# Kernel tuning notes

Hardware: AMD Instinct MI355X
Metric: run time of the kernel (lower is better)

Reference implementation:

```python
import jax, jax.numpy as jnp
import numpy as np

WIN = 9
EPS = 1e-05


def _box_sum(x, win):
    """Depthwise win x win box-filter sum with SAME padding, via two separable 1D convs."""
    C = x.shape[1]
    pad = win // 2
    dn = ('NCHW', 'OIHW', 'NCHW')
    kh = jnp.ones((C, 1, win, 1), dtype=x.dtype)
    kw = jnp.ones((C, 1, 1, win), dtype=x.dtype)
    x = jax.lax.conv_general_dilated(x, kh, (1, 1), [(pad, pad), (0, 0)],
                                     dimension_numbers=dn, feature_group_count=C)
    x = jax.lax.conv_general_dilated(x, kw, (1, 1), [(0, 0), (pad, pad)],
                                     dimension_numbers=dn, feature_group_count=C)
    return x


def setup_inputs() -> dict:
    key = jax.random.key(0)
    k1, k2 = jax.random.split(key)
    B, C, H, W = 32, 4, 512, 512
    y_pred = jax.random.uniform(k1, (B, C, H, W), dtype=jnp.float32)
    y_true = jax.random.uniform(k2, (B, C, H, W), dtype=jnp.float32)
    return {"y_pred": y_pred, "y_true": y_true}


def reference(y_pred, y_true):
    C = y_true.shape[1]
    n = float(WIN * WIN)
    # Stack the 5 moment maps along channels -> one fused box-filter pass.
    stacked = jnp.concatenate(
        [y_true, y_pred, y_true * y_true, y_pred * y_pred, y_true * y_pred], axis=1)
    sums = _box_sum(stacked, WIN)
    sum_I, sum_J, sum_I2, sum_J2, sum_IJ = jnp.split(sums, 5, axis=1)
    mu_I = sum_I / n
    mu_J = sum_J / n
    var_I = sum_I2 / n - mu_I * mu_I
    var_J = sum_J2 / n - mu_J * mu_J
    cov_IJ = sum_IJ / n - mu_I * mu_J
    cc = cov_IJ * cov_IJ / (jnp.maximum(var_I, 0.0) * jnp.maximum(var_J, 0.0) + EPS)
    return -jnp.mean(cc)
```

## Files before the change

### kernel.cpp

```cpp
#include <hip/hip_runtime.h>


#define PAD 4
#define EPS 1e-5f

constexpr int B = 32, C = 4, H = 512, W = 512;
constexpr int ROWS = 32;
constexpr int TPB = 256;
constexpr int CPT = 2;
constexpr int SLOTS = 520;
constexpr int NCHUNK = H / ROWS;
constexpr int NBLK = B * C * NCHUNK;
constexpr int NPART = NBLK * 4;
constexpr float INV_N = 1.0f / 81.0f;

template <bool ADD>
__device__ __forceinline__ void accrow(const float* __restrict__ I,
                                       const float* __restrict__ J,
                                       int r, int x0, float s[5][CPT]) {
    const float2 vi = *(const float2*)(I + (size_t)r * W + x0);
    const float2 vj = *(const float2*)(J + (size_t)r * W + x0);
    float fi[CPT] = {vi.x, vi.y};
    float fj[CPT] = {vj.x, vj.y};
#pragma unroll
    for (int k = 0; k < CPT; ++k) {
        float a = fi[k], b = fj[k];
        if (ADD) {
            s[0][k] += a; s[1][k] += b;
            s[2][k] += a * a; s[3][k] += b * b; s[4][k] += a * b;
        } else {
            s[0][k] -= a; s[1][k] -= b;
            s[2][k] -= a * a; s[3][k] -= b * b; s[4][k] -= a * b;
        }
    }
}

__global__ __launch_bounds__(TPB) void ncc_partial(
        const float* __restrict__ y_pred, const float* __restrict__ y_true,
        float* __restrict__ partial) {
    __shared__ float vs[2][5][SLOTS];

    const int bid = blockIdx.x;
    const int chunk = bid % NCHUNK;
    const int plane = bid / NCHUNK;
    const size_t base = (size_t)plane * H * W;
    const float* I = y_true + base;
    const float* J = y_pred + base;

    const int t = threadIdx.x;
    const int x0 = t * CPT;

    if (t < 2 * PAD) {
        const int sl = (t < PAD) ? t : (512 + t);
#pragma unroll
        for (int b = 0; b < 2; ++b)
#pragma unroll
            for (int ch = 0; ch < 5; ++ch) vs[b][ch][sl] = 0.0f;
    }

    const int y0 = chunk * ROWS;

    float s[5][CPT] = {{0.f, 0.f}, {0.f, 0.f}, {0.f, 0.f}, {0.f, 0.f}, {0.f, 0.f}};

    for (int r = y0 - PAD; r < y0 + PAD; ++r) {
        if (r >= 0 && r < H) accrow<true>(I, J, r, x0, s);
    }

    float acc = 0.0f;

    for (int yo = 0; yo < ROWS; ++yo) {
        const int y = y0 + yo;
        const int rin = y + PAD;
        if (rin < H) accrow<true>(I, J, rin, x0, s);

        float (* const vb)[SLOTS] = vs[yo & 1];
#pragma unroll
        for (int ch = 0; ch < 5; ++ch)
            *(float2*)&vb[ch][x0 + PAD] = make_float2(s[ch][0], s[ch][1]);
        __syncthreads();

        float h[5][CPT];
#pragma unroll
        for (int ch = 0; ch < 5; ++ch) {
            const float* row = vb[ch];
            const float2 r0 = *(const float2*)(row + x0);
            const float2 r1 = *(const float2*)(row + x0 + 2);
            const float2 r2 = *(const float2*)(row + x0 + 4);
            const float2 r3 = *(const float2*)(row + x0 + 6);
            const float2 r4 = *(const float2*)(row + x0 + 8);
            const float s0 = r0.x + r0.y + r1.x + r1.y + r2.x + r2.y +
                             r3.x + r3.y + r4.x;
            h[ch][0] = s0;
            h[ch][1] = s0 + r4.y - r0.x;
        }

#pragma unroll
        for (int k = 0; k < CPT; ++k) {
            const float mI = h[0][k] * INV_N;
            const float mJ = h[1][k] * INV_N;
            const float vI = h[2][k] * INV_N - mI * mI;
            const float vJ = h[3][k] * INV_N - mJ * mJ;
            const float cv = h[4][k] * INV_N - mI * mJ;
            const float den = fmaxf(vI, 0.0f) * fmaxf(vJ, 0.0f) + EPS;
            acc += cv * cv / den;
        }

        const int rout = y - PAD;
        if (rout >= 0) accrow<false>(I, J, rout, x0, s);
    }

#pragma unroll
    for (int off = 32; off > 0; off >>= 1)
        acc += __shfl_down(acc, off, 64);
    if ((t & 63) == 0) partial[bid * 4 + (t >> 6)] = acc;
}

__global__ __launch_bounds__(256) void ncc_final(
        const float* __restrict__ partial, float* __restrict__ out) {
    const int t = threadIdx.x;
    float sum = 0.0f;
    for (int i = t; i < NPART; i += 256) sum += partial[i];
    __shared__ float ws[4];
#pragma unroll
    for (int off = 32; off > 0; off >>= 1)
        sum += __shfl_down(sum, off, 64);
    if ((t & 63) == 0) ws[t >> 6] = sum;
    __syncthreads();
    if (t == 0) {
        const float tot = ws[0] + ws[1] + ws[2] + ws[3];
        out[0] = -tot / (float)((long long)B * C * H * W);
    }
}

extern "C" void kernel_launch(void* const* d_in, const int* in_sizes, int n_in,
                              void* d_out, int out_size, void* d_ws, size_t ws_size,
                              hipStream_t stream) {
    const float* y_pred = (const float*)d_in[0];
    const float* y_true = (const float*)d_in[1];
    float* out = (float*)d_out;
    float* partial = (float*)d_ws;

    ncc_partial<<<NBLK, TPB, 0, stream>>>(y_pred, y_true, partial);
    ncc_final<<<1, 256, 0, stream>>>(partial, out);
}
```

Before: 115.6 us.

## Widen to 4 columns per thread, unroll rows by two with register prefetch

Each thread now handles 4 columns (128 threads per block) using float4 loads. The row loop is unrolled by two with double-buffered shared rows, and the incoming and outgoing rows are prefetched into registers ahead of use to hide global latency. The NCC math is rescaled by 81 to drop divisions and uses a fast reciprocal. Block indices are swizzled, and the per-block partial is reduced to a single value. The approximate reciprocal may slightly change precision, and the larger per-thread register footprint may lower occupancy.

New measurement: 104.0 us. 10.1% less time.

```diff
diff --git a/kernel.cpp b/kernel.cpp
--- a/kernel.cpp
+++ b/kernel.cpp
@@ -2,45 +2,80 @@
 
 
 #define PAD 4
-#define EPS 1e-5f
 
 constexpr int B = 32, C = 4, H = 512, W = 512;
 constexpr int ROWS = 32;
-constexpr int TPB = 256;
-constexpr int CPT = 2;
-constexpr int SLOTS = 520;
+constexpr int TPB = 128;
+constexpr int CPT = 4;
+constexpr int SLOTS = 528;
 constexpr int NCHUNK = H / ROWS;
 constexpr int NBLK = B * C * NCHUNK;
-constexpr int NPART = NBLK * 4;
-constexpr float INV_N = 1.0f / 81.0f;
+constexpr float EPS_N4 = 430.46721f;
 
-template <bool ADD>
-__device__ __forceinline__ void accrow(const float* __restrict__ I,
+struct RowPx { float4 i, j; };
+
+__device__ __forceinline__ void loadpx(const float* __restrict__ I,
                                        const float* __restrict__ J,
-                                       int r, int x0, float s[5][CPT]) {
-    const float2 vi = *(const float2*)(I + (size_t)r * W + x0);
-    const float2 vj = *(const float2*)(J + (size_t)r * W + x0);
-    float fi[CPT] = {vi.x, vi.y};
-    float fj[CPT] = {vj.x, vj.y};
+                                       int r, int x0, RowPx& o) {
+    o.i = *(const float4*)(I + (size_t)r * W + x0);
+    o.j = *(const float4*)(J + (size_t)r * W + x0);
+}
+
+template <int SGN>
+__device__ __forceinline__ void fold4(float s[5][4], const RowPx& R) {
+    const float fi[4] = {R.i.x, R.i.y, R.i.z, R.i.w};
+    const float fj[4] = {R.j.x, R.j.y, R.j.z, R.j.w};
 #pragma unroll
-    for (int k = 0; k < CPT; ++k) {
-        float a = fi[k], b = fj[k];
-        if (ADD) {
-            s[0][k] += a; s[1][k] += b;
-            s[2][k] += a * a; s[3][k] += b * b; s[4][k] += a * b;
+    for (int k = 0; k < 4; ++k) {
+        const float a = fi[k], b = fj[k];
+        if (SGN > 0) {
+            s[0][k] += a;        s[1][k] += b;
+            s[2][k] = fmaf(a, a, s[2][k]);
+            s[3][k] = fmaf(b, b, s[3][k]);
+            s[4][k] = fmaf(a, b, s[4][k]);
         } else {
-            s[0][k] -= a; s[1][k] -= b;
-            s[2][k] -= a * a; s[3][k] -= b * b; s[4][k] -= a * b;
+            s[0][k] -= a;        s[1][k] -= b;
+            s[2][k] = fmaf(-a, a, s[2][k]);
+            s[3][k] = fmaf(-b, b, s[3][k]);
+            s[4][k] = fmaf(-a, b, s[4][k]);
         }
     }
+}
+
+__device__ __forceinline__ float hcc(const float (* __restrict__ vb)[SLOTS],
+                                     const float s[5][4], int x0) {
+    float h[5][4];
+#pragma unroll
+    for (int ch = 0; ch < 5; ++ch) {
+        const float4 L = *(const float4*)&vb[ch][x0];
+        const float4 R = *(const float4*)&vb[ch][x0 + 8];
+        float t = L.x + L.y + L.z + L.w +
+                  s[ch][0] + s[ch][1] + s[ch][2] + s[ch][3] + R.x;
+        h[ch][0] = t;
+        t += R.y - L.x; h[ch][1] = t;
+        t += R.z - L.y; h[ch][2] = t;
+        t += R.w - L.z; h[ch][3] = t;
+    }
+    float acc = 0.0f;
+#pragma unroll
+    for (int k = 0; k < 4; ++k) {
+        const float wi = h[0][k], wj = h[1][k];
+        const float a  = fmaf(81.0f, h[4][k], -(wi * wj));
+        const float vi = fmaxf(fmaf(81.0f, h[2][k], -(wi * wi)), 0.0f);
+        const float vj = fmaxf(fmaf(81.0f, h[3][k], -(wj * wj)), 0.0f);
+        const float den = fmaf(vi, vj, EPS_N4);
+        acc = fmaf(a * a, __builtin_amdgcn_rcpf(den), acc);
+    }
+    return acc;
 }
 
 __global__ __launch_bounds__(TPB) void ncc_partial(
         const float* __restrict__ y_pred, const float* __restrict__ y_true,
         float* __restrict__ partial) {
     __shared__ float vs[2][5][SLOTS];
+    __shared__ float wsum[TPB / 64];
 
-    const int bid = blockIdx.x;
+    const int bid = (blockIdx.x & 7) * (NBLK / 8) + (blockIdx.x >> 3);
     const int chunk = bid % NCHUNK;
     const int plane = bid / NCHUNK;
     const size_t base = (size_t)plane * H * W;
@@ -60,66 +95,73 @@
 
     const int y0 = chunk * ROWS;
 
-    float s[5][CPT] = {{0.f, 0.f}, {0.f, 0.f}, {0.f, 0.f}, {0.f, 0.f}, {0.f, 0.f}};
+    float s[5][4];
+#pragma unroll
+    for (int m = 0; m < 5; ++m)
+#pragma unroll
+        for (int k = 0; k < 4; ++k) s[m][k] = 0.0f;
 
     for (int r = y0 - PAD; r < y0 + PAD; ++r) {
-        if (r >= 0 && r < H) accrow<true>(I, J, r, x0, s);
+        if (r < 0) continue;
+        RowPx R;
+        loadpx(I, J, r, x0, R);
+        fold4<+1>(s, R);
     }
+
+    RowPx A, A2, S, S2, nS2;
+    loadpx(I, J, y0 + PAD, x0, A);
+    loadpx(I, J, y0 + PAD + 1, x0, A2);
+    if (y0 - PAD >= 0) loadpx(I, J, y0 - PAD, x0, S);
+    if (y0 - PAD + 1 >= 0) loadpx(I, J, y0 - PAD + 1, x0, S2);
 
     float acc = 0.0f;
 
-    for (int yo = 0; yo < ROWS; ++yo) {
+    for (int yo = 0; yo < ROWS; yo += 2) {
         const int y = y0 + yo;
-        const int rin = y + PAD;
-        if (rin < H) accrow<true>(I, J, rin, x0, s);
 
-        float (* const vb)[SLOTS] = vs[yo & 1];
+        if (y + PAD < H) fold4<+1>(s, A);
 #pragma unroll
         for (int ch = 0; ch < 5; ++ch)
-            *(float2*)&vb[ch][x0 + PAD] = make_float2(s[ch][0], s[ch][1]);
+            *(float4*)&vs[0][ch][x0 + PAD] =
+                make_float4(s[ch][0], s[ch][1], s[ch][2], s[ch][3]);
+        if (yo + 2 < ROWS && y + 6 < H) loadpx(I, J, y + 6, x0, A);
+
         __syncthreads();
+        acc += hcc(vs[0], s, x0);
 
-        float h[5][CPT];
+        if (y + PAD + 1 < H) fold4<+1>(s, A2);
+        if (y - PAD >= 0)    fold4<-1>(s, S);
 #pragma unroll
-        for (int ch = 0; ch < 5; ++ch) {
-            const float* row = vb[ch];
-            const float2 r0 = *(const float2*)(row + x0);
-            const float2 r1 = *(const float2*)(row + x0 + 2);
-            const float2 r2 = *(const float2*)(row + x0 + 4);
-            const float2 r3 = *(const float2*)(row + x0 + 6);
-            const float2 r4 = *(const float2*)(row + x0 + 8);
-            const float s0 = r0.x + r0.y + r1.x + r1.y + r2.x + r2.y +
-                             r3.x + r3.y + r4.x;
-            h[ch][0] = s0;
-            h[ch][1] = s0 + r4.y - r0.x;
+        for (int ch = 0; ch < 5; ++ch)
+            *(float4*)&vs[1][ch][x0 + PAD] =
+                make_float4(s[ch][0], s[ch][1], s[ch][2], s[ch][3]);
+        if (yo + 2 < ROWS) {
+            if (y + 7 < H)  loadpx(I, J, y + 7, x0, A2);
+            if (y - 2 >= 0) loadpx(I, J, y - 2, x0, S);
+            if (y - 1 >= 0) loadpx(I, J, y - 1, x0, nS2);
         }
 
-#pragma unroll
-        for (int k = 0; k < CPT; ++k) {
-            const float mI = h[0][k] * INV_N;
-            const float mJ = h[1][k] * INV_N;
-            const float vI = h[2][k] * INV_N - mI * mI;
-            const float vJ = h[3][k] * INV_N - mJ * mJ;
-            const float cv = h[4][k] * INV_N - mI * mJ;
-            const float den = fmaxf(vI, 0.0f) * fmaxf(vJ, 0.0f) + EPS;
-            acc += cv * cv / den;
-        }
+        __syncthreads();
+        acc += hcc(vs[1], s, x0);
 
-        const int rout = y - PAD;
-        if (rout >= 0) accrow<false>(I, J, rout, x0, s);
+        if (y - PAD + 1 >= 0) fold4<-1>(s, S2);
+        S2 = nS2;
     }
 
 #pragma unroll
     for (int off = 32; off > 0; off >>= 1)
         acc += __shfl_down(acc, off, 64);
-    if ((t & 63) == 0) partial[bid * 4 + (t >> 6)] = acc;
+    __syncthreads();
+    if ((t & 63) == 0) wsum[t >> 6] = acc;
+    __syncthreads();
+    if (t == 0) partial[bid] = wsum[0] + wsum[1];
 }
 
 __global__ __launch_bounds__(256) void ncc_final(
         const float* __restrict__ partial, float* __restrict__ out) {
     const int t = threadIdx.x;
     float sum = 0.0f;
-    for (int i = t; i < NPART; i += 256) sum += partial[i];
+    for (int i = t; i < NBLK; i += 256) sum += partial[i];
     __shared__ float ws[4];
 #pragma unroll
     for (int off = 32; off > 0; off >>= 1)
```
